# Kernel tuning notes

Hardware: AMD Instinct MI355X
Metric: run time of the kernel (lower is better)

Reference implementation:

```python
import jax, jax.numpy as jnp
import numpy as np

TOP_K = 2  # cfg.MODEL.MOE.TOP_K


def setup_inputs() -> dict:
    key = jax.random.key(0)
    ks = jax.random.split(key, 5)
    bs, L, d_in, d_out, E = 32, 1024, 768, 256, 8
    return {
        "x": jax.random.normal(ks[0], (bs, L, d_in), dtype=jnp.float32),
        "gate_W": jax.random.normal(ks[1], (d_in, E), dtype=jnp.float32) * (1.0 / np.sqrt(d_in)),
        "gate_b": jax.random.normal(ks[2], (E,), dtype=jnp.float32) * 0.01,
        "expert_W": jax.random.normal(ks[3], (E, d_in, d_out), dtype=jnp.float32) * (1.0 / np.sqrt(d_in)),
        "expert_b": jax.random.normal(ks[4], (E, d_out), dtype=jnp.float32) * 0.01,
    }


def reference(x, gate_W, gate_b, expert_W, expert_b):
    # Gate: (bs, L, E) softmax over experts, then top-k routing weights.
    gate_logits = jnp.einsum("bli,ie->ble", x, gate_W) + gate_b
    gate_weights = jax.nn.softmax(gate_logits, axis=-1)
    topk_vals, topk_idx = jax.lax.top_k(gate_weights, TOP_K)  # (bs, L, K)

    # Dense all-expert projection (E is small), then gather the selected ones.
    # all_out: (bs, L, E, d_out)
    all_out = jnp.einsum("bli,eio->bleo", x, expert_W) + expert_b

    # Select top-k expert outputs per token: (bs, L, K, d_out)
    sel = jnp.take_along_axis(all_out, topk_idx[..., None], axis=2)

    # Weighted combine over the K routed experts -> (bs, L, d_out)
    output = jnp.sum(sel * topk_vals[..., None], axis=2)
    return output
```

## Files before the change

### kernel.cpp

```cpp
#include <hip/hip_runtime.h>
#include <hip/hip_bf16.h>
#include <stdint.h>

#define T_TOKENS 32768
#define D_IN     768
#define D_OUT    256
#define N_EXP    8
#define S_TOT    (T_TOKENS*2)
#define S_PAD    66048

typedef __attribute__((ext_vector_type(8))) short bf16x8;
typedef __attribute__((ext_vector_type(4))) float f32x4;

__device__ __forceinline__ unsigned short f2bf(float f) {
    unsigned u = __float_as_uint(f);
    return (unsigned short)((u + 0x7FFFu + ((u >> 16) & 1u)) >> 16);
}
__device__ __forceinline__ unsigned pack_bf2(float a, float b) {
    return (unsigned)f2bf(a) | ((unsigned)f2bf(b) << 16);
}

__device__ __forceinline__ void async16(void* lds, const void* g) {
    __builtin_amdgcn_global_load_lds(
        (const __attribute__((address_space(1))) unsigned int*)g,
        (__attribute__((address_space(3))) unsigned int*)lds, 16, 0, 0);
}

__global__ void convw_kernel(const float* __restrict__ W, unsigned short* __restrict__ WT) {
    int idx = blockIdx.x * 256 + threadIdx.x;
    float v = W[idx];
    int n  = idx & 255;
    int ek = idx >> 8;
    int k  = ek % D_IN;
    int e  = ek / D_IN;
    WT[(size_t)e * (D_IN * D_OUT) + (size_t)n * D_IN + k] = f2bf(v);
}

__global__ __launch_bounds__(64) void gate_partial_kernel(
        const float* __restrict__ x, const float* __restrict__ gW,
        unsigned short* __restrict__ xbf, float* __restrict__ partial) {
    __shared__ float tile[64 * 65];
    int tid = threadIdx.x;
    int t0  = blockIdx.x * 64;
    int kq  = blockIdx.y;
    int c16 = tid & 15, rb = tid >> 4;
    float acc[8] = {0,0,0,0,0,0,0,0};
    #pragma unroll 1
    for (int j = 0; j < 3; j++) {
        int kc = kq * 192 + j * 64;
        #pragma unroll
        for (int i = 0; i < 16; i++) {
            int row = i * 4 + rb;
            size_t g = (size_t)(t0 + row) * D_IN + kc + c16 * 4;
            float4 v = *(const float4*)(x + g);
            uint2 p; p.x = pack_bf2(v.x, v.y); p.y = pack_bf2(v.z, v.w);
            *(uint2*)(xbf + g) = p;
            float* d = &tile[row * 65 + c16 * 4];
            d[0] = v.x; d[1] = v.y; d[2] = v.z; d[3] = v.w;
        }
        __syncthreads();
        const float* gr = gW + (size_t)kc * 8;
        #pragma unroll 8
        for (int kk = 0; kk < 64; kk++) {
            float xv = tile[tid * 65 + kk];
            #pragma unroll
            for (int e = 0; e < 8; e++) acc[e] += xv * gr[kk * 8 + e];
        }
        __syncthreads();
    }
    float* dst = partial + ((size_t)kq * T_TOKENS + t0 + tid) * 8;
    float4 o0 = {acc[0], acc[1], acc[2], acc[3]};
    float4 o1 = {acc[4], acc[5], acc[6], acc[7]};
    *(float4*)dst = o0; *(float4*)(dst + 4) = o1;
}

__global__ __launch_bounds__(256) void gate_final_kernel(
        const float* __restrict__ partial, const float* __restrict__ gb,
        float* __restrict__ topk_w, int* __restrict__ topk_e, int* __restrict__ counts) {
    __shared__ int h[8];
    int tid = threadIdx.x;
    if (tid < 8) h[tid] = 0;
    __syncthreads();
    int t = blockIdx.x * 256 + tid;
    float acc[8] = {0,0,0,0,0,0,0,0};
    #pragma unroll
    for (int q = 0; q < 4; q++) {
        const float* p = partial + ((size_t)q * T_TOKENS + t) * 8;
        float4 a = *(const float4*)p;
        float4 b = *(const float4*)(p + 4);
        acc[0] += a.x; acc[1] += a.y; acc[2] += a.z; acc[3] += a.w;
        acc[4] += b.x; acc[5] += b.y; acc[6] += b.z; acc[7] += b.w;
    }
    float mx = -1e30f;
    #pragma unroll
    for (int e = 0; e < 8; e++) { acc[e] += gb[e]; mx = fmaxf(mx, acc[e]); }
    float w[8], s = 0.f;
    #pragma unroll
    for (int e = 0; e < 8; e++) { w[e] = expf(acc[e] - mx); s += w[e]; }
    float inv = 1.0f / s;
    int e0 = 0; float b0 = -1.f;
    #pragma unroll
    for (int e = 0; e < 8; e++) if (w[e] > b0) { b0 = w[e]; e0 = e; }
    int e1 = 0; float b1 = -1.f;
    #pragma unroll
    for (int e = 0; e < 8; e++) if (e != e0 && w[e] > b1) { b1 = w[e]; e1 = e; }
    topk_w[t*2]   = b0 * inv;
    topk_w[t*2+1] = b1 * inv;
    topk_e[t*2]   = e0;
    topk_e[t*2+1] = e1;
    atomicAdd(&h[e0], 1); atomicAdd(&h[e1], 1);
    __syncthreads();
    if (tid < 8) atomicAdd(&counts[tid], h[tid]);
}

__global__ void scatter_kernel(const int* __restrict__ topk_e, const float* __restrict__ topk_w,
                               const int* __restrict__ counts, int* __restrict__ cursors,
                               int* __restrict__ slot_token, float* __restrict__ slot_w,
                               int* __restrict__ inv_slot) {
    int offs[9]; offs[0] = 0;
    #pragma unroll
    for (int e = 0; e < 8; e++) offs[e+1] = offs[e] + ((counts[e] + 63) & ~63);
    __shared__ int hcnt[8], hbase[8];
    if (threadIdx.x < 8) hcnt[threadIdx.x] = 0;
    __syncthreads();
    int idx[4], ee[4], lr[4];
    int base = blockIdx.x * 256 * 4 + threadIdx.x;
    #pragma unroll
    for (int j = 0; j < 4; j++) {
        idx[j] = base + j * 256;
        ee[j]  = topk_e[idx[j]];
        lr[j]  = atomicAdd(&hcnt[ee[j]], 1);
    }
    __syncthreads();
    if (threadIdx.x < 8) hbase[threadIdx.x] = atomicAdd(&cursors[threadIdx.x], hcnt[threadIdx.x]);
    __syncthreads();
    #pragma unroll
    for (int j = 0; j < 4; j++) {
        int slot = offs[ee[j]] + hbase[ee[j]] + lr[j];
        slot_token[slot] = idx[j] >> 1;
        slot_w[slot]     = topk_w[idx[j]];
        inv_slot[idx[j]] = slot;
    }
}

template<bool ROUTED>
__global__ __launch_bounds__(256, 4) void moe_gemm_kernel(
        const unsigned short* __restrict__ xbf, const unsigned short* __restrict__ WT,
        const float* __restrict__ eb, const int* __restrict__ counts,
        const int* __restrict__ slot_token, const float* __restrict__ slot_w,
        float* __restrict__ dst) {
    __shared__ unsigned short A_lds[2][64 * 32];
    __shared__ unsigned short B_lds[2][256 * 32];

    int offs[9]; offs[0] = 0;
    #pragma unroll
    for (int e = 0; e < 8; e++) offs[e+1] = offs[e] + ((counts[e] + 63) & ~63);
    int row0 = blockIdx.x * 64;
    if (row0 >= offs[8]) return;
    int expert = 0;
    #pragma unroll
    for (int e = 0; e < 8; e++) if (row0 >= offs[e]) expert = e;

    int tid  = threadIdx.x;
    int wave = tid >> 6, lane = tid & 63;
    int lrow = lane & 15, lquad = lane >> 4;

    int srow = tid >> 2;
    int pch  = tid & 3;
    int lc_a = (pch - (srow >> 1)) & 3;
    int tokA = slot_token[row0 + srow];
    const unsigned short* abase = xbf + (size_t)tokA * D_IN + lc_a * 8;

    const unsigned short* bb = WT + (size_t)expert * (D_IN * D_OUT);
    const unsigned short* bsrc[4];
    #pragma unroll
    for (int i = 0; i < 4; i++) {
        int ci = i * 256 + tid;
        int br = ci >> 2, bp = ci & 3;
        int lc = (bp - (br >> 1)) & 3;
        bsrc[i] = bb + (size_t)br * D_IN + lc * 8;
    }

    int a_off[4], b_off[4];
    #pragma unroll
    for (int m = 0; m < 4; m++) {
        int r = m * 16 + lrow;
        a_off[m] = r * 32 + ((lquad + (r >> 1)) & 3) * 8;
    }
    #pragma unroll
    for (int s = 0; s < 4; s++) {
        int r = wave * 64 + s * 16 + lrow;
        b_off[s] = r * 32 + ((lquad + (r >> 1)) & 3) * 8;
    }

    f32x4 acc[4][4];
    #pragma unroll
    for (int m = 0; m < 4; m++)
        #pragma unroll
        for (int s = 0; s < 4; s++) acc[m][s] = (f32x4){0,0,0,0};

    auto stage = [&](int k0, int p) {
        async16(&A_lds[p][tid * 8], abase + k0);
        #pragma unroll
        for (int i = 0; i < 4; i++) async16(&B_lds[p][(i * 256 + tid) * 8], bsrc[i] + k0);
    };

    stage(0, 0);
    #pragma unroll 1
    for (int s = 0; s < D_IN / 32; s++) {
        __syncthreads();
        if (s < D_IN / 32 - 1) stage((s + 1) * 32, (s + 1) & 1);
        int p = s & 1;
        bf16x8 a[4];
        #pragma unroll
        for (int m = 0; m < 4; m++) a[m] = *(const bf16x8*)&A_lds[p][a_off[m]];
        #pragma unroll
        for (int q = 0; q < 4; q++) {
            bf16x8 b = *(const bf16x8*)&B_lds[p][b_off[q]];
            #pragma unroll
            for (int m = 0; m < 4; m++)
                acc[m][q] = __builtin_amdgcn_mfma_f32_16x16x32_bf16(a[m], b, acc[m][q], 0, 0, 0);
        }
    }

    float bias_s[4];
    #pragma unroll
    for (int q = 0; q < 4; q++) bias_s[q] = eb[expert * D_OUT + wave * 64 + q * 16 + lrow];
    #pragma unroll
    for (int m = 0; m < 4; m++) {
        #pragma unroll
        for (int r = 0; r < 4; r++) {
            int slot = row0 + m * 16 + lquad * 4 + r;
            if constexpr (ROUTED) {
                float* drow = dst + (size_t)slot * D_OUT;
                #pragma unroll
                for (int q = 0; q < 4; q++)
                    drow[wave * 64 + q * 16 + lrow] = acc[m][q][r] + bias_s[q];
            } else {
                int tk = slot_token[slot];
                float wgt = slot_w[slot];
                #pragma unroll
                for (int q = 0; q < 4; q++)
                    atomicAdd(dst + (size_t)tk * D_OUT + wave * 64 + q * 16 + lrow,
                              wgt * (acc[m][q][r] + bias_s[q]));
            }
        }
    }
}

__global__ void combine_kernel(const float* __restrict__ routed, const int* __restrict__ inv_slot,
                               const float* __restrict__ topk_w, float* __restrict__ out) {
    int flat = blockIdx.x * 256 + threadIdx.x;
    int t = flat >> 6, c = (flat & 63) * 4;
    int   s0 = inv_slot[t*2], s1 = inv_slot[t*2+1];
    float w0 = topk_w[t*2],   w1 = topk_w[t*2+1];
    float4 r0 = *(const float4*)(routed + (size_t)s0 * D_OUT + c);
    float4 r1 = *(const float4*)(routed + (size_t)s1 * D_OUT + c);
    float4 o;
    o.x = w0*r0.x + w1*r1.x; o.y = w0*r0.y + w1*r1.y;
    o.z = w0*r0.z + w1*r1.z; o.w = w0*r0.w + w1*r1.w;
    *(float4*)(out + (size_t)t * D_OUT + c) = o;
}

extern "C" void kernel_launch(void* const* d_in, const int* in_sizes, int n_in,
                              void* d_out, int out_size, void* d_ws, size_t ws_size,
                              hipStream_t stream) {
    const float* x  = (const float*)d_in[0];
    const float* gW = (const float*)d_in[1];
    const float* gb = (const float*)d_in[2];
    const float* eW = (const float*)d_in[3];
    const float* eb = (const float*)d_in[4];
    float* out = (float*)d_out;
    char* ws = (char*)d_ws;

    float* topk_w      = (float*)(ws + 0);
    int*   topk_e      = (int*)  (ws + 262144);
    int*   counts      = (int*)  (ws + 524288);
    int*   cursors     = (int*)  (ws + 524320);
    int*   slot_token  = (int*)  (ws + 524416);
    float* slot_w      = (float*)(ws + 788608);
    int*   inv_slot    = (int*)  (ws + 1052800);
    float* partial     = (float*)(ws + 1314944);
    unsigned short* WT = (unsigned short*)(ws + 5509248);
    unsigned short* xbf= (unsigned short*)(ws + 8654976);
    float* routed      = (float*)(ws + 58986624);
    const size_t NEED_ROUTED = 58986624 + (size_t)S_PAD * D_OUT * 4;
    bool use_routed = (ws_size >= NEED_ROUTED);

    hipMemsetAsync(ws + 524288, 0, 128, stream);
    hipMemsetAsync(slot_token, 0, 528384, stream);

    convw_kernel       <<<N_EXP * D_IN * D_OUT / 256, 256, 0, stream>>>(eW, WT);
    gate_partial_kernel<<<dim3(T_TOKENS / 64, 4), 64, 0, stream>>>(x, gW, xbf, partial);
    gate_final_kernel  <<<T_TOKENS / 256, 256, 0, stream>>>(partial, gb, topk_w, topk_e, counts);
    scatter_kernel     <<<S_TOT / (256 * 4), 256, 0, stream>>>(topk_e, topk_w, counts, cursors,
                                                               slot_token, slot_w, inv_slot);
    if (use_routed) {
        moe_gemm_kernel<true><<<S_PAD / 64, 256, 0, stream>>>(xbf, WT, eb, counts,
                                                              slot_token, slot_w, routed);
        combine_kernel<<<T_TOKENS * D_OUT / 4 / 256, 256, 0, stream>>>(routed, inv_slot,
                                                                       topk_w, out);
    } else {
        hipMemsetAsync(out, 0, (size_t)out_size * sizeof(float), stream);
        moe_gemm_kernel<false><<<S_PAD / 64, 256, 0, stream>>>(xbf, WT, eb, counts,
                                                               slot_token, slot_w, out);
    }
}
```

Baseline: 274.2 us.

## Enlarge MoE GEMM tile to 128 rows, split gate K six ways, drop memsets

The grouped expert GEMM now covers 128 routed rows per block instead of 64, with padding rounded up to 128. Each B (weight) tile loaded into LDS is therefore reused across twice as many rows, at the cost of more accumulator registers and an occupancy target lowered to 2. The gate partial kernel splits K into six chunks for more parallelism. The counts/cursors memset moves into the weight-conversion kernel, and the slot_token memset is dropped on the routed path, with token indices clamped instead, so fewer launches are needed.

```diff
diff --git a/kernel.cpp b/kernel.cpp
--- a/kernel.cpp
+++ b/kernel.cpp
@@ -7,7 +7,8 @@
 #define D_OUT    256
 #define N_EXP    8
 #define S_TOT    (T_TOKENS*2)
-#define S_PAD    66048
+#define S_PAD    66560
+#define KSPLIT   6
 
 typedef __attribute__((ext_vector_type(8))) short bf16x8;
 typedef __attribute__((ext_vector_type(4))) float f32x4;
@@ -26,7 +27,9 @@
         (__attribute__((address_space(3))) unsigned int*)lds, 16, 0, 0);
 }
 
-__global__ void convw_kernel(const float* __restrict__ W, unsigned short* __restrict__ WT) {
+__global__ void convw_kernel(const float* __restrict__ W, unsigned short* __restrict__ WT,
+                             int* __restrict__ zero16) {
+    if (blockIdx.x == 0 && threadIdx.x < 16) zero16[threadIdx.x] = 0;
     int idx = blockIdx.x * 256 + threadIdx.x;
     float v = W[idx];
     int n  = idx & 255;
@@ -46,8 +49,8 @@
     int c16 = tid & 15, rb = tid >> 4;
     float acc[8] = {0,0,0,0,0,0,0,0};
     #pragma unroll 1
-    for (int j = 0; j < 3; j++) {
-        int kc = kq * 192 + j * 64;
+    for (int j = 0; j < 2; j++) {
+        int kc = kq * 128 + j * 64;
         #pragma unroll
         for (int i = 0; i < 16; i++) {
             int row = i * 4 + rb;
@@ -84,7 +87,7 @@
     int t = blockIdx.x * 256 + tid;
     float acc[8] = {0,0,0,0,0,0,0,0};
     #pragma unroll
-    for (int q = 0; q < 4; q++) {
+    for (int q = 0; q < KSPLIT; q++) {
         const float* p = partial + ((size_t)q * T_TOKENS + t) * 8;
         float4 a = *(const float4*)p;
         float4 b = *(const float4*)(p + 4);
@@ -119,7 +122,7 @@
                                int* __restrict__ inv_slot) {
     int offs[9]; offs[0] = 0;
     #pragma unroll
-    for (int e = 0; e < 8; e++) offs[e+1] = offs[e] + ((counts[e] + 63) & ~63);
+    for (int e = 0; e < 8; e++) offs[e+1] = offs[e] + ((counts[e] + 127) & ~127);
     __shared__ int hcnt[8], hbase[8];
     if (threadIdx.x < 8) hcnt[threadIdx.x] = 0;
     __syncthreads();
@@ -144,18 +147,18 @@
 }
 
 template<bool ROUTED>
-__global__ __launch_bounds__(256, 4) void moe_gemm_kernel(
+__global__ __launch_bounds__(256, 2) void moe_gemm_kernel(
         const unsigned short* __restrict__ xbf, const unsigned short* __restrict__ WT,
         const float* __restrict__ eb, const int* __restrict__ counts,
         const int* __restrict__ slot_token, const float* __restrict__ slot_w,
         float* __restrict__ dst) {
-    __shared__ unsigned short A_lds[2][64 * 32];
+    __shared__ unsigned short A_lds[2][128 * 32];
     __shared__ unsigned short B_lds[2][256 * 32];
 
     int offs[9]; offs[0] = 0;
     #pragma unroll
-    for (int e = 0; e < 8; e++) offs[e+1] = offs[e] + ((counts[e] + 63) & ~63);
-    int row0 = blockIdx.x * 64;
+    for (int e = 0; e < 8; e++) offs[e+1] = offs[e] + ((counts[e] + 127) & ~127);
+    int row0 = blockIdx.x * 128;
     if (row0 >= offs[8]) return;
     int expert = 0;
     #pragma unroll
@@ -165,42 +168,47 @@
     int wave = tid >> 6, lane = tid & 63;
     int lrow = lane & 15, lquad = lane >> 4;
 
-    int srow = tid >> 2;
-    int pch  = tid & 3;
-    int lc_a = (pch - (srow >> 1)) & 3;
-    int tokA = slot_token[row0 + srow];
-    const unsigned short* abase = xbf + (size_t)tokA * D_IN + lc_a * 8;
-
+    const unsigned short* asrc[2];
+    #pragma unroll
+    for (int i = 0; i < 2; i++) {
+        int c = i * 256 + tid;
+        int r = c >> 2, p = c & 3;
+        int lc = (p - (r >> 1)) & 3;
+        int tok = slot_token[row0 + r];
+        tok = tok < 0 ? 0 : (tok >= T_TOKENS ? 0 : tok);
+        asrc[i] = xbf + (size_t)tok * D_IN + lc * 8;
+    }
     const unsigned short* bb = WT + (size_t)expert * (D_IN * D_OUT);
     const unsigned short* bsrc[4];
     #pragma unroll
     for (int i = 0; i < 4; i++) {
-        int ci = i * 256 + tid;
-        int br = ci >> 2, bp = ci & 3;
-        int lc = (bp - (br >> 1)) & 3;
-        bsrc[i] = bb + (size_t)br * D_IN + lc * 8;
-    }
-
-    int a_off[4], b_off[4];
-    #pragma unroll
-    for (int m = 0; m < 4; m++) {
+        int c = i * 256 + tid;
+        int r = c >> 2, p = c & 3;
+        int lc = (p - (r >> 1)) & 3;
+        bsrc[i] = bb + (size_t)r * D_IN + lc * 8;
+    }
+
+    int a_off[8], b_off[4];
+    #pragma unroll
+    for (int m = 0; m < 8; m++) {
         int r = m * 16 + lrow;
         a_off[m] = r * 32 + ((lquad + (r >> 1)) & 3) * 8;
     }
     #pragma unroll
-    for (int s = 0; s < 4; s++) {
-        int r = wave * 64 + s * 16 + lrow;
-        b_off[s] = r * 32 + ((lquad + (r >> 1)) & 3) * 8;
-    }
-
-    f32x4 acc[4][4];
-    #pragma unroll
-    for (int m = 0; m < 4; m++)
-        #pragma unroll
-        for (int s = 0; s < 4; s++) acc[m][s] = (f32x4){0,0,0,0};
+    for (int q = 0; q < 4; q++) {
+        int r = wave * 64 + q * 16 + lrow;
+        b_off[q] = r * 32 + ((lquad + (r >> 1)) & 3) * 8;
+    }
+
+    f32x4 acc[8][4];
+    #pragma unroll
+    for (int m = 0; m < 8; m++)
+        #pragma unroll
+        for (int q = 0; q < 4; q++) acc[m][q] = (f32x4){0,0,0,0};
 
     auto stage = [&](int k0, int p) {
-        async16(&A_lds[p][tid * 8], abase + k0);
+        #pragma unroll
+        for (int i = 0; i < 2; i++) async16(&A_lds[p][(i * 256 + tid) * 8], asrc[i] + k0);
         #pragma unroll
         for (int i = 0; i < 4; i++) async16(&B_lds[p][(i * 256 + tid) * 8], bsrc[i] + k0);
     };
@@ -211,38 +219,38 @@
         __syncthreads();
         if (s < D_IN / 32 - 1) stage((s + 1) * 32, (s + 1) & 1);
         int p = s & 1;
-        bf16x8 a[4];
-        #pragma unroll
-        for (int m = 0; m < 4; m++) a[m] = *(const bf16x8*)&A_lds[p][a_off[m]];
+        bf16x8 a[8];
+        #pragma unroll
+        for (int m = 0; m < 8; m++) a[m] = *(const bf16x8*)&A_lds[p][a_off[m]];
         #pragma unroll
         for (int q = 0; q < 4; q++) {
             bf16x8 b = *(const bf16x8*)&B_lds[p][b_off[q]];
             #pragma unroll
-            for (int m = 0; m < 4; m++)
+            for (int m = 0; m < 8; m++)
                 acc[m][q] = __builtin_amdgcn_mfma_f32_16x16x32_bf16(a[m], b, acc[m][q], 0, 0, 0);
         }
     }
 
-    float bias_s[4];
-    #pragma unroll
-    for (int q = 0; q < 4; q++) bias_s[q] = eb[expert * D_OUT + wave * 64 + q * 16 + lrow];
-    #pragma unroll
-    for (int m = 0; m < 4; m++) {
+    float bias_q[4];
+    #pragma unroll
+    for (int q = 0; q < 4; q++) bias_q[q] = eb[expert * D_OUT + wave * 64 + q * 16 + lrow];
+    #pragma unroll
+    for (int m = 0; m < 8; m++) {
         #pragma unroll
         for (int r = 0; r < 4; r++) {
             int slot = row0 + m * 16 + lquad * 4 + r;
             if constexpr (ROUTED) {
-                float* drow = dst + (size_t)slot * D_OUT;
+                float* drow = dst + (size_t)slot * D_OUT + wave * 64;
                 #pragma unroll
                 for (int q = 0; q < 4; q++)
-                    drow[wave * 64 + q * 16 + lrow] = acc[m][q][r] + bias_s[q];
+                    drow[q * 16 + lrow] = acc[m][q][r] + bias_q[q];
             } else {
                 int tk = slot_token[slot];
                 float wgt = slot_w[slot];
                 #pragma unroll
                 for (int q = 0; q < 4; q++)
                     atomicAdd(dst + (size_t)tk * D_OUT + wave * 64 + q * 16 + lrow,
-                              wgt * (acc[m][q][r] + bias_s[q]));
+                              wgt * (acc[m][q][r] + bias_q[q]));
             }
         }
     }
@@ -278,31 +286,29 @@
     int*   counts      = (int*)  (ws + 524288);
     int*   cursors     = (int*)  (ws + 524320);
     int*   slot_token  = (int*)  (ws + 524416);
-    float* slot_w      = (float*)(ws + 788608);
-    int*   inv_slot    = (int*)  (ws + 1052800);
-    float* partial     = (float*)(ws + 1314944);
-    unsigned short* WT = (unsigned short*)(ws + 5509248);
-    unsigned short* xbf= (unsigned short*)(ws + 8654976);
-    float* routed      = (float*)(ws + 58986624);
-    const size_t NEED_ROUTED = 58986624 + (size_t)S_PAD * D_OUT * 4;
+    float* slot_w      = (float*)(ws + 790656);
+    int*   inv_slot    = (int*)  (ws + 1056896);
+    float* partial     = (float*)(ws + 1319040);
+    unsigned short* WT = (unsigned short*)(ws + 7610496);
+    unsigned short* xbf= (unsigned short*)(ws + 10756224);
+    float* routed      = (float*)(ws + 61087872);
+    const size_t NEED_ROUTED = 61087872 + (size_t)S_PAD * D_OUT * 4;
     bool use_routed = (ws_size >= NEED_ROUTED);
 
-    hipMemsetAsync(ws + 524288, 0, 128, stream);
-    hipMemsetAsync(slot_token, 0, 528384, stream);
-
-    convw_kernel       <<<N_EXP * D_IN * D_OUT / 256, 256, 0, stream>>>(eW, WT);
-    gate_partial_kernel<<<dim3(T_TOKENS / 64, 4), 64, 0, stream>>>(x, gW, xbf, partial);
+    convw_kernel       <<<N_EXP * D_IN * D_OUT / 256, 256, 0, stream>>>(eW, WT, counts);
+    gate_partial_kernel<<<dim3(T_TOKENS / 64, KSPLIT), 64, 0, stream>>>(x, gW, xbf, partial);
     gate_final_kernel  <<<T_TOKENS / 256, 256, 0, stream>>>(partial, gb, topk_w, topk_e, counts);
     scatter_kernel     <<<S_TOT / (256 * 4), 256, 0, stream>>>(topk_e, topk_w, counts, cursors,
                                                                slot_token, slot_w, inv_slot);
     if (use_routed) {
-        moe_gemm_kernel<true><<<S_PAD / 64, 256, 0, stream>>>(xbf, WT, eb, counts,
-                                                              slot_token, slot_w, routed);
+        moe_gemm_kernel<true><<<S_PAD / 128, 256, 0, stream>>>(xbf, WT, eb, counts,
+                                                               slot_token, slot_w, routed);
         combine_kernel<<<T_TOKENS * D_OUT / 4 / 256, 256, 0, stream>>>(routed, inv_slot,
                                                                        topk_w, out);
     } else {
+        hipMemsetAsync(slot_token, 0, 532480, stream);
         hipMemsetAsync(out, 0, (size_t)out_size * sizeof(float), stream);
-        moe_gemm_kernel<false><<<S_PAD / 64, 256, 0, stream>>>(xbf, WT, eb, counts,
-                                                               slot_token, slot_w, out);
-    }
-}
+        moe_gemm_kernel<false><<<S_PAD / 128, 256, 0, stream>>>(xbf, WT, eb, counts,
+                                                                slot_token, slot_w, out);
+    }
+}
```

New measurement: 271.7 us. Within noise of the previous version (-0.9%).
